# Kernel optimization log

Hardware: AMD Instinct MI355X
Metric: run time of the kernel (lower is better)

Reference implementation:

```python
import jax, jax.numpy as jnp
import numpy as np
from jax import lax

DIM = 1024      # model dim
DS = 16         # d_state
DC = 4          # d_conv
EXP = 2
DI = DIM * EXP  # d_inner = 2048
B, L = 2, 1024


def setup_inputs() -> dict:
    key = jax.random.key(0)
    ks = jax.random.split(key, 10)
    s = lambda k, shape, sc: jax.random.normal(k, shape, jnp.float32) * sc
    return {
        "x": s(ks[0], (B, L, DIM), 1.0),
        "norm_w": jnp.ones((DIM,), jnp.float32),
        "norm_b": jnp.zeros((DIM,), jnp.float32),
        "in_proj_w": s(ks[1], (2 * DI, DIM), DIM ** -0.5),
        "conv_w": s(ks[2], (DI, 1, DC), DC ** -0.5),   # depthwise: (out=DI, in/groups=1, K)
        "conv_b": jnp.zeros((DI,), jnp.float32),
        "x_proj_w": s(ks[3], (2 * DS + 1, DI), DI ** -0.5),
        "dt_w": s(ks[4], (DI, 1), 1.0),
        "dt_b": jax.random.uniform(ks[5], (DI,), jnp.float32, -0.001, 0.001),
        "A_log": s(ks[6], (DI, DS), 1.0),              # self.A (randn); A = -exp(A_log)
        "D_skip": jnp.ones((DI,), jnp.float32),
        "out_proj_w": s(ks[7], (DIM, DI), DI ** -0.5),
    }


def _ssm(x, x_proj_w, dt_w, dt_b, A_log, D_skip):
    # x: (B, L, DI)
    xp = jnp.einsum('bli,pi->blp', x, x_proj_w)            # (B, L, 2*DS+1)
    delta = jax.nn.softplus(xp[..., :1] * dt_w[:, 0] + dt_b)  # (B, L, DI)
    Bp = xp[..., 1:DS + 1]                                  # (B, L, DS)
    Cp = xp[..., DS + 1:]                                   # (B, L, DS)
    A = -jnp.exp(A_log)                                     # (DI, DS)
    dA = jnp.exp(delta[..., None] * A)                      # (B, L, DI, DS)
    dB = delta[..., None] * Bp[:, :, None, :] * x[..., None]  # (B, L, DI, DS)

    def step(h, inp):
        dA_t, dB_t, C_t = inp                               # (B,DI,DS),(B,DI,DS),(B,DS)
        h = dA_t * h + dB_t
        return h, jnp.einsum('bdn,bn->bd', h, C_t)

    h0 = jnp.zeros((x.shape[0], DI, DS), x.dtype)
    _, ys = lax.scan(step, h0, (jnp.swapaxes(dA, 0, 1),
                                jnp.swapaxes(dB, 0, 1),
                                jnp.swapaxes(Cp, 0, 1)))
    y = jnp.swapaxes(ys, 0, 1)                              # (B, L, DI)
    return y + x * D_skip


def reference(x, norm_w, norm_b, in_proj_w, conv_w, conv_b,
              x_proj_w, dt_w, dt_b, A_log, D_skip, out_proj_w):
    # LayerNorm
    mu = x.mean(-1, keepdims=True)
    var = ((x - mu) ** 2).mean(-1, keepdims=True)
    xn = (x - mu) * lax.rsqrt(var + 1e-5) * norm_w + norm_b
    # input projection and gate split
    xz = jnp.einsum('bld,pd->blp', xn, in_proj_w)           # (B, L, 2*DI)
    xi, z = xz[..., :DI], xz[..., DI:]
    # causal depthwise conv (torch pads K-1 both sides then slices [:L] == left-pad K-1)
    xc = lax.conv_general_dilated(jnp.swapaxes(xi, 1, 2), conv_w, (1,),
                                  [(DC - 1, 0)], feature_group_count=DI,
                                  dimension_numbers=('NCH', 'OIH', 'NCH'))
    xc = jnp.swapaxes(xc + conv_b[None, :, None], 1, 2)     # (B, L, DI)
    xc = jax.nn.silu(xc)
    y = _ssm(xc, x_proj_w, dt_w, dt_b, A_log, D_skip)
    y = y * jax.nn.silu(z)
    return x + jnp.einsum('bli,di->bld', y, out_proj_w)
```

## Files before the change

### kernel.cpp

```cpp
#include <hip/hip_runtime.h>
#include <stdint.h>

#define BATCH 2
#define SEQ   1024
#define DIM_  1024
#define DS_   16
#define DI_   2048
#define NTOK  (BATCH*SEQ)
#define NSEG  32
#define LSEG  (SEQ/NSEG)

typedef unsigned short u16;
using s16x8 = __attribute__((ext_vector_type(8))) short;
using f32x4 = __attribute__((ext_vector_type(4))) float;
using u16x4 = __attribute__((ext_vector_type(4))) unsigned short;
using u16x8 = __attribute__((ext_vector_type(8))) unsigned short;

__device__ __forceinline__ float bf2f(u16 u) {
  union { unsigned int i; float f; } c; c.i = ((unsigned int)u) << 16; return c.f;
}
__device__ __forceinline__ u16 f2bf(float f) {
  union { float f; unsigned int i; } c; c.f = f;
  unsigned int r = c.i + 0x7fffu + ((c.i >> 16) & 1u);
  return (u16)(r >> 16);
}
__device__ __forceinline__ float softplus_f(float x) {
  return (x > 15.f) ? x : __logf(1.f + __expf(x));
}
__device__ __forceinline__ u16x4 f4_to_bf(float4 v) {
  u16x4 r; r[0] = f2bf(v.x); r[1] = f2bf(v.y); r[2] = f2bf(v.z); r[3] = f2bf(v.w);
  return r;
}

#define N4_INW  (2 * DI_ * DIM_ / 4)
#define N4_OUTW (DIM_ * DI_ / 4)
#define CVT_BLOCKS ((N4_INW + N4_OUTW + 32768) / 256)
__global__ __launch_bounds__(256) void cvt_ln_kernel(const float* __restrict__ in_w,
    const float* __restrict__ out_w, const float* __restrict__ xproj_w,
    const float* __restrict__ x, const float* __restrict__ nw,
    const float* __restrict__ nb, u16* __restrict__ in_w_bf,
    u16* __restrict__ out_w_bf, u16* __restrict__ xpw_bf, u16* __restrict__ xn) {
  int tid = threadIdx.x;
  if (blockIdx.x < CVT_BLOCKS) {
    int i = blockIdx.x * 256 + tid;
    if (i < N4_INW) {
      ((u16x4*)in_w_bf)[i] = f4_to_bf(((const float4*)in_w)[i]);
    } else if (i < N4_INW + N4_OUTW) {
      int j = i - N4_INW;
      ((u16x4*)out_w_bf)[j] = f4_to_bf(((const float4*)out_w)[j]);
    } else {
      int j = i - (N4_INW + N4_OUTW);
      if (j >= 32768) return;
      int p = (j * 4) >> 11;
      u16x4 r;
      if (p < 33) r = f4_to_bf(((const float4*)xproj_w)[j]);
      else { r[0] = 0; r[1] = 0; r[2] = 0; r[3] = 0; }
      ((u16x4*)xpw_bf)[j] = r;
    }
    return;
  }
  int t = blockIdx.x - CVT_BLOCKS;
  const float* row = x + (size_t)t * DIM_;
  float4 v = ((const float4*)row)[tid];
  float f[4] = {v.x, v.y, v.z, v.w};
  float s = 0.f, sq = 0.f;
#pragma unroll
  for (int j = 0; j < 4; j++) { s += f[j]; sq += f[j] * f[j]; }
#pragma unroll
  for (int m = 1; m < 64; m <<= 1) { s += __shfl_xor(s, m); sq += __shfl_xor(sq, m); }
  __shared__ float rs_[4], rq_[4];
  int wv = tid >> 6;
  if ((tid & 63) == 0) { rs_[wv] = s; rq_[wv] = sq; }
  __syncthreads();
  s = rs_[0] + rs_[1] + rs_[2] + rs_[3];
  sq = rq_[0] + rq_[1] + rq_[2] + rq_[3];
  float mu = s * (1.0f / DIM_);
  float var = sq * (1.0f / DIM_) - mu * mu;
  float rstd = rsqrtf(var + 1e-5f);
  float4 wn = ((const float4*)nw)[tid];
  float4 bn = ((const float4*)nb)[tid];
  u16x4 o;
  o[0] = f2bf((f[0] - mu) * rstd * wn.x + bn.x);
  o[1] = f2bf((f[1] - mu) * rstd * wn.y + bn.y);
  o[2] = f2bf((f[2] - mu) * rstd * wn.z + bn.z);
  o[3] = f2bf((f[3] - mu) * rstd * wn.w + bn.w);
  *(u16x4*)(xn + (size_t)t * DIM_ + tid * 4) = o;
}

template<int TBM, int TBN, int BK, typename OUT, int EPI, int KSPLIT = 1, int SWZ = 0>
__global__ __launch_bounds__(256) void gemm_bt(const u16* __restrict__ A,
    const u16* __restrict__ Wt, OUT* __restrict__ C, const float* __restrict__ X,
    int M, int N, int K) {
  constexpr int LDT = BK + 8;
  constexpr int TPR = BK / 8;
  constexpr int RPP = 256 / TPR;
  constexpr int ALn = TBM / RPP;
  constexpr int BLn = TBN / RPP;
  constexpr int KK = BK / 32;
  constexpr int WM = TBM / 2, WN = TBN / 2;
  constexpr int MI = WM / 16, NJ = WN / 16;
  __shared__ __align__(16) u16 sA[TBM * LDT];
  __shared__ __align__(16) u16 sB[TBN * LDT];
  const int tid = threadIdx.x;
  const int lane = tid & 63, wv = tid >> 6;
  const int wm = (wv >> 1) * WM, wn = (wv & 1) * WN;
  const int bxl = SWZ ? ((blockIdx.x & 7) * (gridDim.x >> 3) + (blockIdx.x >> 3))
                      : blockIdx.x;
  const int bm0 = blockIdx.y * TBM, bn0 = bxl * TBN;
  const int q = lane >> 4, r16 = lane & 15;
  const int srow = tid / TPR, scol = (tid % TPR) * 8;
  const int kc = K / KSPLIT;
  const int k0 = (KSPLIT > 1) ? blockIdx.z * kc : 0;
  const int kend = k0 + kc;

  f32x4 acc[MI][NJ];
#pragma unroll
  for (int i = 0; i < MI; i++)
#pragma unroll
    for (int j = 0; j < NJ; j++)
#pragma unroll
      for (int r = 0; r < 4; r++) acc[i][j][r] = 0.f;

  const u16* Ag = A + (size_t)bm0 * K + scol + k0;
  const u16* Wg = Wt + (size_t)bn0 * K + scol + k0;
  s16x8 ra[ALn], rb[BLn];
#pragma unroll
  for (int i = 0; i < ALn; i++) ra[i] = *(const s16x8*)(Ag + (size_t)(srow + i * RPP) * K);
#pragma unroll
  for (int i = 0; i < BLn; i++) rb[i] = *(const s16x8*)(Wg + (size_t)(srow + i * RPP) * K);

  for (int kt = k0; kt < kend; kt += BK) {
    __syncthreads();
#pragma unroll
    for (int i = 0; i < ALn; i++) *(s16x8*)&sA[(srow + i * RPP) * LDT + scol] = ra[i];
#pragma unroll
    for (int i = 0; i < BLn; i++) *(s16x8*)&sB[(srow + i * RPP) * LDT + scol] = rb[i];
    __syncthreads();
    int kn = kt + BK - k0;
    if (kn < kc) {
#pragma unroll
      for (int i = 0; i < ALn; i++) ra[i] = *(const s16x8*)(Ag + (size_t)(srow + i * RPP) * K + kn);
#pragma unroll
      for (int i = 0; i < BLn; i++) rb[i] = *(const s16x8*)(Wg + (size_t)(srow + i * RPP) * K + kn);
    }
#pragma unroll
    for (int kk = 0; kk < KK; kk++) {
      s16x8 fa[MI], fb[NJ];
#pragma unroll
      for (int i = 0; i < MI; i++)
        fa[i] = *(const s16x8*)&sA[(wm + i * 16 + r16) * LDT + kk * 32 + q * 8];
#pragma unroll
      for (int j = 0; j < NJ; j++)
        fb[j] = *(const s16x8*)&sB[(wn + j * 16 + r16) * LDT + kk * 32 + q * 8];
#pragma unroll
      for (int i = 0; i < MI; i++)
#pragma unroll
        for (int j = 0; j < NJ; j++)
          acc[i][j] = __builtin_amdgcn_mfma_f32_16x16x32_bf16(fa[i], fb[j], acc[i][j], 0, 0, 0);
    }
  }
  OUT* Cz = C + ((KSPLIT > 1) ? (size_t)blockIdx.z * M * N : 0);
#pragma unroll
  for (int i = 0; i < MI; i++)
#pragma unroll
    for (int j = 0; j < NJ; j++) {
      int row0 = bm0 + wm + i * 16 + q * 4;
      int col = bn0 + wn + j * 16 + r16;
#pragma unroll
      for (int r = 0; r < 4; r++) {
        size_t off = (size_t)(row0 + r) * N + col;
        float v = acc[i][j][r];
        if constexpr (EPI == 1) v += X[off];
        if constexpr (sizeof(OUT) == 2) Cz[off] = f2bf(v);
        else                            Cz[off] = v;
      }
    }
}

__global__ __launch_bounds__(256) void conv_silu_kernel(const u16* __restrict__ xz,
    const float* __restrict__ cw, const float* __restrict__ cb, u16* __restrict__ xc) {
  int t = blockIdx.x;
  int l = t & (SEQ - 1);
  int c0 = threadIdx.x * 8;
  float acc[8], wk[8][4];
#pragma unroll
  for (int j = 0; j < 8; j++) {
    float4 wv = ((const float4*)cw)[c0 + j];
    wk[j][0] = wv.x; wk[j][1] = wv.y; wk[j][2] = wv.z; wk[j][3] = wv.w;
    acc[j] = cb[c0 + j];
  }
#pragma unroll
  for (int k = 0; k < 4; k++) {
    int lk = l - 3 + k;
    if (lk >= 0) {
      u16x8 v = *(const u16x8*)(xz + (size_t)(t - 3 + k) * (2 * DI_) + c0);
#pragma unroll
      for (int j = 0; j < 8; j++) acc[j] = fmaf(bf2f(v[j]), wk[j][k], acc[j]);
    }
  }
  u16x8 o;
#pragma unroll
  for (int j = 0; j < 8; j++) {
    float a = acc[j];
    o[j] = f2bf(a / (1.0f + __expf(-a)));
  }
  *(u16x8*)(xc + (size_t)t * DI_ + c0) = o;
}

__global__ __launch_bounds__(256) void xp_finish_kernel(const float* __restrict__ part,
    const float* __restrict__ dtw, const float* __restrict__ dtb,
    u16* __restrict__ xz, float* __restrict__ bc) {
  int t = blockIdx.x;
  int tid = threadIdx.x;
  __shared__ float xps[64];
  if (tid < 64) {
    float s = 0.f;
#pragma unroll
    for (int k = 0; k < 8; k++)
      s += part[(size_t)k * NTOK * 64 + (size_t)t * 64 + tid];
    xps[tid] = s;
  }
  __syncthreads();
  if (tid < 32) bc[(size_t)t * 32 + tid] = xps[1 + tid];
  float dr = xps[0];
  int c0 = tid * 8;
  float wv[8], bv[8];
  *(float4*)wv = ((const float4*)(dtw + c0))[0];
  *(float4*)(wv + 4) = ((const float4*)(dtw + c0))[1];
  *(float4*)bv = ((const float4*)(dtb + c0))[0];
  *(float4*)(bv + 4) = ((const float4*)(dtb + c0))[1];
  u16x8 o;
#pragma unroll
  for (int j = 0; j < 8; j++) o[j] = f2bf(softplus_f(dr * wv[j] + bv[j]));
  *(u16x8*)(xz + (size_t)t * (2 * DI_) + c0) = o;
}

#define SRT 72
#define SBC 36

__global__ __launch_bounds__(256) void scan_pass1(const float* __restrict__ bc,
    const u16* __restrict__ dlt, const u16* __restrict__ xc,
    const float* __restrict__ A_log, float* __restrict__ P, float* __restrict__ Q) {
  __shared__ __align__(16) u16 sD[LSEG * SRT];
  __shared__ __align__(16) u16 sX[LSEG * SRT];
  __shared__ __align__(16) float sB[LSEG * SBC];
  int tid = threadIdx.x;
  int lane = tid & 63, wv = tid >> 6;
  int nl = (lane & 3) * 4;
  int dl = wv * 16 + (lane >> 2);
  int d0 = blockIdx.x * 64;
  int s = blockIdx.y, b = blockIdx.z;
  int t0 = b * SEQ + s * LSEG;
  {
    int tr = tid >> 3, c = (tid & 7) * 8;
    *(u16x8*)&sD[tr * SRT + c] = *(const u16x8*)(dlt + (size_t)(t0 + tr) * (2 * DI_) + d0 + c);
    *(u16x8*)&sX[tr * SRT + c] = *(const u16x8*)(xc  + (size_t)(t0 + tr) * DI_ + d0 + c);
    int tb = tid & 31, cb = (tid >> 5) * 4;
    *(f32x4*)&sB[tb * SBC + cb] = *(const f32x4*)(bc + (size_t)(t0 + tb) * 32 + cb);
  }
  int d = d0 + dl;
  float4 Ain = *(const float4*)(A_log + d * DS_ + nl);
  f32x4 Av;
  Av[0] = -__expf(Ain.x); Av[1] = -__expf(Ain.y);
  Av[2] = -__expf(Ain.z); Av[3] = -__expf(Ain.w);
  f32x4 Pv, h;
#pragma unroll
  for (int i = 0; i < 4; i++) { Pv[i] = 1.f; h[i] = 0.f; }
  __syncthreads();
#pragma unroll 8
  for (int j = 0; j < LSEG; j++) {
    float delta = bf2f(sD[j * SRT + dl]);
    float xcv   = bf2f(sX[j * SRT + dl]);
    f32x4 B4 = *(const f32x4*)&sB[j * SBC + nl];
    float du = delta * xcv;
#pragma unroll
    for (int i = 0; i < 4; i++) {
      float a = __expf(delta * Av[i]);
      Pv[i] *= a;
      h[i] = fmaf(a, h[i], du * B4[i]);
    }
  }
  size_t idx = ((size_t)((b * NSEG + s) * DI_ + d)) * 16 + nl;
  *(f32x4*)(P + idx) = Pv;
  *(f32x4*)(Q + idx) = h;
}

__global__ __launch_bounds__(256) void scan_combine(const float* __restrict__ P,
    float* __restrict__ Q) {
  int g = blockIdx.x * 256 + threadIdx.x;
  int n = g & 15, d = (g >> 4) & (DI_ - 1), b = g >> 15;
  size_t base = ((size_t)b * NSEG * DI_ + d) * 16 + n;
  constexpr size_t STR = (size_t)DI_ * 16;
  float p_[NSEG], q_[NSEG];
#pragma unroll
  for (int s = 0; s < NSEG; s++) {
    p_[s] = P[base + s * STR];
    q_[s] = Q[base + s * STR];
  }
  float hh = 0.f;
#pragma unroll
  for (int s = 0; s < NSEG; s++) {
    Q[base + s * STR] = hh;
    hh = fmaf(p_[s], hh, q_[s]);
  }
}

__global__ __launch_bounds__(256) void scan_pass2(const float* __restrict__ bc,
    const u16* __restrict__ dlt, const u16* __restrict__ xc,
    const float* __restrict__ A_log, const float* __restrict__ Dskip,
    const float* __restrict__ Hin, u16* __restrict__ yb) {
  __shared__ __align__(16) u16 sD[LSEG * SRT];
  __shared__ __align__(16) u16 sX[LSEG * SRT];
  __shared__ __align__(16) u16 sZ[LSEG * SRT];
  __shared__ __align__(16) float sB[LSEG * SBC];
  int tid = threadIdx.x;
  int lane = tid & 63, wv = tid >> 6;
  int nl = (lane & 3) * 4;
  int dl = wv * 16 + (lane >> 2);
  int d0 = blockIdx.x * 64;
  int s = blockIdx.y, b = blockIdx.z;
  int t0 = b * SEQ + s * LSEG;
  {
    int tr = tid >> 3, c = (tid & 7) * 8;
    *(u16x8*)&sD[tr * SRT + c] = *(const u16x8*)(dlt + (size_t)(t0 + tr) * (2 * DI_) + d0 + c);
    *(u16x8*)&sZ[tr * SRT + c] = *(const u16x8*)(dlt + (size_t)(t0 + tr) * (2 * DI_) + DI_ + d0 + c);
    *(u16x8*)&sX[tr * SRT + c] = *(const u16x8*)(xc  + (size_t)(t0 + tr) * DI_ + d0 + c);
    int tb = tid & 31, cb = (tid >> 5) * 4;
    *(f32x4*)&sB[tb * SBC + cb] = *(const f32x4*)(bc + (size_t)(t0 + tb) * 32 + cb);
  }
  int d = d0 + dl;
  float4 Ain = *(const float4*)(A_log + d * DS_ + nl);
  f32x4 Av;
  Av[0] = -__expf(Ain.x); Av[1] = -__expf(Ain.y);
  Av[2] = -__expf(Ain.z); Av[3] = -__expf(Ain.w);
  float Dv = Dskip[d];
  size_t idx = ((size_t)((b * NSEG + s) * DI_ + d)) * 16 + nl;
  f32x4 h = *(const f32x4*)(Hin + idx);
  __syncthreads();
#pragma unroll 8
  for (int j = 0; j < LSEG; j++) {
    float delta = bf2f(sD[j * SRT + dl]);
    float xcv   = bf2f(sX[j * SRT + dl]);
    f32x4 B4 = *(const f32x4*)&sB[j * SBC + nl];
    f32x4 C4 = *(const f32x4*)&sB[j * SBC + 16 + nl];
    float du = delta * xcv;
#pragma unroll
    for (int i = 0; i < 4; i++) {
      float a = __expf(delta * Av[i]);
      h[i] = fmaf(a, h[i], du * B4[i]);
    }
    float p = h[0] * C4[0];
    p = fmaf(h[1], C4[1], p);
    p = fmaf(h[2], C4[2], p);
    p = fmaf(h[3], C4[3], p);
    p += __shfl_xor(p, 1);
    p += __shfl_xor(p, 2);
    if ((lane & 3) == 0) {
      float z = bf2f(sZ[j * SRT + dl]);
      float sz = z / (1.0f + __expf(-z));
      yb[(size_t)(t0 + j) * DI_ + d] = f2bf((p + xcv * Dv) * sz);
    }
  }
}

extern "C" void kernel_launch(void* const* d_in, const int* in_sizes, int n_in,
                              void* d_out, int out_size, void* d_ws, size_t ws_size,
                              hipStream_t stream) {
  const float* x      = (const float*)d_in[0];
  const float* norm_w = (const float*)d_in[1];
  const float* norm_b = (const float*)d_in[2];
  const float* in_w   = (const float*)d_in[3];
  const float* conv_w = (const float*)d_in[4];
  const float* conv_b = (const float*)d_in[5];
  const float* xproj_w= (const float*)d_in[6];
  const float* dt_w   = (const float*)d_in[7];
  const float* dt_b   = (const float*)d_in[8];
  const float* A_log  = (const float*)d_in[9];
  const float* D_skip = (const float*)d_in[10];
  const float* out_w  = (const float*)d_in[11];
  float* out = (float*)d_out;

  char* ws = (char*)d_ws;
  size_t off = 0;
  auto alloc = [&](size_t bytes) { void* p = ws + off; off += (bytes + 255) & ~255ULL; return p; };
  u16* in_w_bf  = (u16*)alloc((size_t)2 * DI_ * DIM_ * 2);
  u16* out_w_bf = (u16*)alloc((size_t)DIM_ * DI_ * 2);
  u16* xpw_bf   = (u16*)alloc((size_t)64 * DI_ * 2);
  u16* xn       = (u16*)alloc((size_t)NTOK * DIM_ * 2);
  u16* xz       = (u16*)alloc((size_t)NTOK * 2 * DI_ * 2);
  u16* xc       = (u16*)alloc((size_t)NTOK * DI_ * 2);
  float* bc     = (float*)alloc((size_t)NTOK * 32 * 4);
  float* xp_part= (float*)alloc((size_t)8 * NTOK * 64 * 4);
  float* P      = (float*)alloc((size_t)BATCH * NSEG * DI_ * 16 * 4);
  float* Q      = (float*)alloc((size_t)BATCH * NSEG * DI_ * 16 * 4);
  u16* yb       = (u16*)alloc((size_t)NTOK * DI_ * 2);

  cvt_ln_kernel<<<CVT_BLOCKS + NTOK, 256, 0, stream>>>(in_w, out_w, xproj_w, x,
                                                       norm_w, norm_b, in_w_bf,
                                                       out_w_bf, xpw_bf, xn);
  gemm_bt<128, 128, 64, u16, 0, 1, 1><<<dim3((2 * DI_) / 128, NTOK / 128), 256, 0, stream>>>(
      xn, in_w_bf, xz, nullptr, NTOK, 2 * DI_, DIM_);
  conv_silu_kernel<<<NTOK, 256, 0, stream>>>(xz, conv_w, conv_b, xc);
  gemm_bt<64, 64, 32, float, 0, 8><<<dim3(1, NTOK / 64, 8), 256, 0, stream>>>(
      xc, xpw_bf, xp_part, nullptr, NTOK, 64, DI_);
  xp_finish_kernel<<<NTOK, 256, 0, stream>>>(xp_part, dt_w, dt_b, xz, bc);
  scan_pass1<<<dim3(DI_ / 64, NSEG, BATCH), 256, 0, stream>>>(bc, xz, xc, A_log, P, Q);
  scan_combine<<<BATCH * DI_ * 16 / 256, 256, 0, stream>>>(P, Q);
  scan_pass2<<<dim3(DI_ / 64, NSEG, BATCH), 256, 0, stream>>>(bc, xz, xc, A_log, D_skip,
                                                              Q, yb);
  gemm_bt<64, 64, 64, float, 1, 1, 1><<<dim3(DIM_ / 64, NTOK / 64), 256, 0, stream>>>(
      yb, out_w_bf, out, x, NTOK, DIM_, DI_);
}
```

Measured before the change: 224.6 us.

## Fuse x_proj partial reduction and delta softplus into scan passes; transpose P/Q layout

Removes the separate xp_finish kernel. Both scan passes now sum the split-K x_proj partials for their token segment themselves and compute softplus delta directly into shared memory, so the bc and delta buffers are never written to or read back from global memory. The P/Q carry layout is changed to segment-contiguous so scan_combine reads and writes contiguous runs instead of large strides. In exchange, the partial sums and softplus are computed redundantly by each d-block, and the stores in pass1 become scattered.

```diff
diff --git a/kernel.cpp b/kernel.cpp
--- a/kernel.cpp
+++ b/kernel.cpp
@@ -207,43 +207,18 @@
   *(u16x8*)(xc + (size_t)t * DI_ + c0) = o;
 }
 
-__global__ __launch_bounds__(256) void xp_finish_kernel(const float* __restrict__ part,
-    const float* __restrict__ dtw, const float* __restrict__ dtb,
-    u16* __restrict__ xz, float* __restrict__ bc) {
-  int t = blockIdx.x;
-  int tid = threadIdx.x;
-  __shared__ float xps[64];
-  if (tid < 64) {
-    float s = 0.f;
-#pragma unroll
-    for (int k = 0; k < 8; k++)
-      s += part[(size_t)k * NTOK * 64 + (size_t)t * 64 + tid];
-    xps[tid] = s;
-  }
-  __syncthreads();
-  if (tid < 32) bc[(size_t)t * 32 + tid] = xps[1 + tid];
-  float dr = xps[0];
-  int c0 = tid * 8;
-  float wv[8], bv[8];
-  *(float4*)wv = ((const float4*)(dtw + c0))[0];
-  *(float4*)(wv + 4) = ((const float4*)(dtw + c0))[1];
-  *(float4*)bv = ((const float4*)(dtb + c0))[0];
-  *(float4*)(bv + 4) = ((const float4*)(dtb + c0))[1];
-  u16x8 o;
-#pragma unroll
-  for (int j = 0; j < 8; j++) o[j] = f2bf(softplus_f(dr * wv[j] + bv[j]));
-  *(u16x8*)(xz + (size_t)t * (2 * DI_) + c0) = o;
-}
-
 #define SRT 72
 #define SBC 36
 
-__global__ __launch_bounds__(256) void scan_pass1(const float* __restrict__ bc,
-    const u16* __restrict__ dlt, const u16* __restrict__ xc,
-    const float* __restrict__ A_log, float* __restrict__ P, float* __restrict__ Q) {
+
+__global__ __launch_bounds__(256) void scan_pass1(const float* __restrict__ part,
+    const float* __restrict__ dtw, const float* __restrict__ dtb,
+    const u16* __restrict__ xc, const float* __restrict__ A_log,
+    float* __restrict__ P, float* __restrict__ Q) {
   __shared__ __align__(16) u16 sD[LSEG * SRT];
   __shared__ __align__(16) u16 sX[LSEG * SRT];
-  __shared__ __align__(16) float sB[LSEG * SBC];
+  __shared__ __align__(16) float sBC[LSEG * SBC];
+  __shared__ float sDr[LSEG];
   int tid = threadIdx.x;
   int lane = tid & 63, wv = tid >> 6;
   int nl = (lane & 3) * 4;
@@ -251,12 +226,49 @@
   int d0 = blockIdx.x * 64;
   int s = blockIdx.y, b = blockIdx.z;
   int t0 = b * SEQ + s * LSEG;
+  int tr = tid >> 3;
   {
-    int tr = tid >> 3, c = (tid & 7) * 8;
-    *(u16x8*)&sD[tr * SRT + c] = *(const u16x8*)(dlt + (size_t)(t0 + tr) * (2 * DI_) + d0 + c);
-    *(u16x8*)&sX[tr * SRT + c] = *(const u16x8*)(xc  + (size_t)(t0 + tr) * DI_ + d0 + c);
-    int tb = tid & 31, cb = (tid >> 5) * 4;
-    *(f32x4*)&sB[tb * SBC + cb] = *(const f32x4*)(bc + (size_t)(t0 + tb) * 32 + cb);
+    int c = (tid & 7) * 8;
+    *(u16x8*)&sX[tr * SRT + c] = *(const u16x8*)(xc + (size_t)(t0 + tr) * DI_ + d0 + c);
+    int pg = tid & 7;
+    if (pg < 5) {
+      int pc = pg * 8;
+      float v[8];
+#pragma unroll
+      for (int j = 0; j < 8; j++) v[j] = 0.f;
+#pragma unroll
+      for (int k = 0; k < 8; k++) {
+        const float* pp = part + ((size_t)k * NTOK + (t0 + tr)) * 64 + pc;
+        float4 a0 = *(const float4*)pp;
+        float4 a1 = *(const float4*)(pp + 4);
+        v[0] += a0.x; v[1] += a0.y; v[2] += a0.z; v[3] += a0.w;
+        v[4] += a1.x; v[5] += a1.y; v[6] += a1.z; v[7] += a1.w;
+      }
+#pragma unroll
+      for (int j = 0; j < 8; j++) {
+        int p = pc + j;
+        if (p == 0) sDr[tr] = v[j];
+        else if (p <= 32) sBC[tr * SBC + (p - 1)] = v[j];
+      }
+    }
+  }
+  __syncthreads();
+  {
+    int dc = (tid & 7) * 8;
+    float dr = sDr[tr];
+    float4 w0 = *(const float4*)(dtw + d0 + dc);
+    float4 w1 = *(const float4*)(dtw + d0 + dc + 4);
+    float4 b0 = *(const float4*)(dtb + d0 + dc);
+    float4 b1 = *(const float4*)(dtb + d0 + dc + 4);
+    u16* sp = &sD[tr * SRT + dc];
+    sp[0] = f2bf(softplus_f(dr * w0.x + b0.x));
+    sp[1] = f2bf(softplus_f(dr * w0.y + b0.y));
+    sp[2] = f2bf(softplus_f(dr * w0.z + b0.z));
+    sp[3] = f2bf(softplus_f(dr * w0.w + b0.w));
+    sp[4] = f2bf(softplus_f(dr * w1.x + b1.x));
+    sp[5] = f2bf(softplus_f(dr * w1.y + b1.y));
+    sp[6] = f2bf(softplus_f(dr * w1.z + b1.z));
+    sp[7] = f2bf(softplus_f(dr * w1.w + b1.w));
   }
   int d = d0 + dl;
   float4 Ain = *(const float4*)(A_log + d * DS_ + nl);
@@ -271,7 +283,7 @@
   for (int j = 0; j < LSEG; j++) {
     float delta = bf2f(sD[j * SRT + dl]);
     float xcv   = bf2f(sX[j * SRT + dl]);
-    f32x4 B4 = *(const f32x4*)&sB[j * SBC + nl];
+    f32x4 B4 = *(const f32x4*)&sBC[j * SBC + nl];
     float du = delta * xcv;
 #pragma unroll
     for (int i = 0; i < 4; i++) {
@@ -280,39 +292,42 @@
       h[i] = fmaf(a, h[i], du * B4[i]);
     }
   }
-  size_t idx = ((size_t)((b * NSEG + s) * DI_ + d)) * 16 + nl;
-  *(f32x4*)(P + idx) = Pv;
-  *(f32x4*)(Q + idx) = h;
+  size_t base = ((size_t)(b * DI_ + d) * 16 + nl) * NSEG + s;
+#pragma unroll
+  for (int i = 0; i < 4; i++) {
+    P[base + (size_t)i * NSEG] = Pv[i];
+    Q[base + (size_t)i * NSEG] = h[i];
+  }
 }
 
 __global__ __launch_bounds__(256) void scan_combine(const float* __restrict__ P,
     float* __restrict__ Q) {
   int g = blockIdx.x * 256 + threadIdx.x;
-  int n = g & 15, d = (g >> 4) & (DI_ - 1), b = g >> 15;
-  size_t base = ((size_t)b * NSEG * DI_ + d) * 16 + n;
-  constexpr size_t STR = (size_t)DI_ * 16;
+  size_t base = (size_t)g * NSEG;
   float p_[NSEG], q_[NSEG];
 #pragma unroll
   for (int s = 0; s < NSEG; s++) {
-    p_[s] = P[base + s * STR];
-    q_[s] = Q[base + s * STR];
+    p_[s] = P[base + s];
+    q_[s] = Q[base + s];
   }
   float hh = 0.f;
 #pragma unroll
   for (int s = 0; s < NSEG; s++) {
-    Q[base + s * STR] = hh;
+    Q[base + s] = hh;
     hh = fmaf(p_[s], hh, q_[s]);
   }
 }
 
-__global__ __launch_bounds__(256) void scan_pass2(const float* __restrict__ bc,
-    const u16* __restrict__ dlt, const u16* __restrict__ xc,
+__global__ __launch_bounds__(256) void scan_pass2(const float* __restrict__ part,
+    const float* __restrict__ dtw, const float* __restrict__ dtb,
+    const u16* __restrict__ xz, const u16* __restrict__ xc,
     const float* __restrict__ A_log, const float* __restrict__ Dskip,
     const float* __restrict__ Hin, u16* __restrict__ yb) {
   __shared__ __align__(16) u16 sD[LSEG * SRT];
   __shared__ __align__(16) u16 sX[LSEG * SRT];
   __shared__ __align__(16) u16 sZ[LSEG * SRT];
-  __shared__ __align__(16) float sB[LSEG * SBC];
+  __shared__ __align__(16) float sBC[LSEG * SBC];
+  __shared__ float sDr[LSEG];
   int tid = threadIdx.x;
   int lane = tid & 63, wv = tid >> 6;
   int nl = (lane & 3) * 4;
@@ -320,13 +335,50 @@
   int d0 = blockIdx.x * 64;
   int s = blockIdx.y, b = blockIdx.z;
   int t0 = b * SEQ + s * LSEG;
+  int tr = tid >> 3;
   {
-    int tr = tid >> 3, c = (tid & 7) * 8;
-    *(u16x8*)&sD[tr * SRT + c] = *(const u16x8*)(dlt + (size_t)(t0 + tr) * (2 * DI_) + d0 + c);
-    *(u16x8*)&sZ[tr * SRT + c] = *(const u16x8*)(dlt + (size_t)(t0 + tr) * (2 * DI_) + DI_ + d0 + c);
-    *(u16x8*)&sX[tr * SRT + c] = *(const u16x8*)(xc  + (size_t)(t0 + tr) * DI_ + d0 + c);
-    int tb = tid & 31, cb = (tid >> 5) * 4;
-    *(f32x4*)&sB[tb * SBC + cb] = *(const f32x4*)(bc + (size_t)(t0 + tb) * 32 + cb);
+    int c = (tid & 7) * 8;
+    *(u16x8*)&sX[tr * SRT + c] = *(const u16x8*)(xc + (size_t)(t0 + tr) * DI_ + d0 + c);
+    *(u16x8*)&sZ[tr * SRT + c] = *(const u16x8*)(xz + (size_t)(t0 + tr) * (2 * DI_) + DI_ + d0 + c);
+    int pg = tid & 7;
+    if (pg < 5) {
+      int pc = pg * 8;
+      float v[8];
+#pragma unroll
+      for (int j = 0; j < 8; j++) v[j] = 0.f;
+#pragma unroll
+      for (int k = 0; k < 8; k++) {
+        const float* pp = part + ((size_t)k * NTOK + (t0 + tr)) * 64 + pc;
+        float4 a0 = *(const float4*)pp;
+        float4 a1 = *(const float4*)(pp + 4);
+        v[0] += a0.x; v[1] += a0.y; v[2] += a0.z; v[3] += a0.w;
+        v[4] += a1.x; v[5] += a1.y; v[6] += a1.z; v[7] += a1.w;
+      }
+#pragma unroll
+      for (int j = 0; j < 8; j++) {
+        int p = pc + j;
+        if (p == 0) sDr[tr] = v[j];
+        else if (p <= 32) sBC[tr * SBC + (p - 1)] = v[j];
+      }
+    }
+  }
+  __syncthreads();
+  {
+    int dc = (tid & 7) * 8;
+    float dr = sDr[tr];
+    float4 w0 = *(const float4*)(dtw + d0 + dc);
+    float4 w1 = *(const float4*)(dtw + d0 + dc + 4);
+    float4 b0 = *(const float4*)(dtb + d0 + dc);
+    float4 b1 = *(const float4*)(dtb + d0 + dc + 4);
+    u16* sp = &sD[tr * SRT + dc];
+    sp[0] = f2bf(softplus_f(dr * w0.x + b0.x));
+    sp[1] = f2bf(softplus_f(dr * w0.y + b0.y));
+    sp[2] = f2bf(softplus_f(dr * w0.z + b0.z));
+    sp[3] = f2bf(softplus_f(dr * w0.w + b0.w));
+    sp[4] = f2bf(softplus_f(dr * w1.x + b1.x));
+    sp[5] = f2bf(softplus_f(dr * w1.y + b1.y));
+    sp[6] = f2bf(softplus_f(dr * w1.z + b1.z));
+    sp[7] = f2bf(softplus_f(dr * w1.w + b1.w));
   }
   int d = d0 + dl;
   float4 Ain = *(const float4*)(A_log + d * DS_ + nl);
@@ -334,15 +386,17 @@
   Av[0] = -__expf(Ain.x); Av[1] = -__expf(Ain.y);
   Av[2] = -__expf(Ain.z); Av[3] = -__expf(Ain.w);
   float Dv = Dskip[d];
-  size_t idx = ((size_t)((b * NSEG + s) * DI_ + d)) * 16 + nl;
-  f32x4 h = *(const f32x4*)(Hin + idx);
+  size_t hbase = ((size_t)(b * DI_ + d) * 16 + nl) * NSEG + s;
+  f32x4 h;
+#pragma unroll
+  for (int i = 0; i < 4; i++) h[i] = Hin[hbase + (size_t)i * NSEG];
   __syncthreads();
 #pragma unroll 8
   for (int j = 0; j < LSEG; j++) {
     float delta = bf2f(sD[j * SRT + dl]);
     float xcv   = bf2f(sX[j * SRT + dl]);
-    f32x4 B4 = *(const f32x4*)&sB[j * SBC + nl];
-    f32x4 C4 = *(const f32x4*)&sB[j * SBC + 16 + nl];
+    f32x4 B4 = *(const f32x4*)&sBC[j * SBC + nl];
+    f32x4 C4 = *(const f32x4*)&sBC[j * SBC + 16 + nl];
     float du = delta * xcv;
 #pragma unroll
     for (int i = 0; i < 4; i++) {
@@ -389,7 +443,6 @@
   u16* xn       = (u16*)alloc((size_t)NTOK * DIM_ * 2);
   u16* xz       = (u16*)alloc((size_t)NTOK * 2 * DI_ * 2);
   u16* xc       = (u16*)alloc((size_t)NTOK * DI_ * 2);
-  float* bc     = (float*)alloc((size_t)NTOK * 32 * 4);
   float* xp_part= (float*)alloc((size_t)8 * NTOK * 64 * 4);
   float* P      = (float*)alloc((size_t)BATCH * NSEG * DI_ * 16 * 4);
   float* Q      = (float*)alloc((size_t)BATCH * NSEG * DI_ * 16 * 4);
@@ -403,10 +456,11 @@
   conv_silu_kernel<<<NTOK, 256, 0, stream>>>(xz, conv_w, conv_b, xc);
   gemm_bt<64, 64, 32, float, 0, 8><<<dim3(1, NTOK / 64, 8), 256, 0, stream>>>(
       xc, xpw_bf, xp_part, nullptr, NTOK, 64, DI_);
-  xp_finish_kernel<<<NTOK, 256, 0, stream>>>(xp_part, dt_w, dt_b, xz, bc);
-  scan_pass1<<<dim3(DI_ / 64, NSEG, BATCH), 256, 0, stream>>>(bc, xz, xc, A_log, P, Q);
+  scan_pass1<<<dim3(DI_ / 64, NSEG, BATCH), 256, 0, stream>>>(xp_part, dt_w, dt_b,
+                                                              xc, A_log, P, Q);
   scan_combine<<<BATCH * DI_ * 16 / 256, 256, 0, stream>>>(P, Q);
-  scan_pass2<<<dim3(DI_ / 64, NSEG, BATCH), 256, 0, stream>>>(bc, xz, xc, A_log, D_skip,
+  scan_pass2<<<dim3(DI_ / 64, NSEG, BATCH), 256, 0, stream>>>(xp_part, dt_w, dt_b,
+                                                              xz, xc, A_log, D_skip,
                                                               Q, yb);
   gemm_bt<64, 64, 64, float, 1, 1, 1><<<dim3(DIM_ / 64, NTOK / 64), 256, 0, stream>>>(
       yb, out_w_bf, out, x, NTOK, DIM_, DI_);
```

After: 242.1 us. 1.08x slower.
